# Kernel optimization log

Hardware: AMD Instinct MI355X
Metric: run time of the kernel (lower is better)

The kernel has to match this reference:

```python
import jax, jax.numpy as jnp
import numpy as np

N_NODES = 100000
IN_C, HID_C, OUT_C = 128, 128, 64
N_EDGES, N_POS, N_NEG = 1600000, 200000, 200000
BN_EPS = 1e-5


def setup_inputs() -> dict:
    key = jax.random.key(0)
    ks = jax.random.split(key, 24)
    s = 0.05
    inp = {
        'x': jax.random.normal(ks[0], (N_NODES, IN_C), jnp.float32),
        'edge_index': jax.random.randint(ks[1], (2, N_EDGES), 0, N_NODES, jnp.int64 if jax.config.jax_enable_x64 else jnp.int32),
        'pos_edge_index': jax.random.randint(ks[2], (2, N_POS), 0, N_NODES, jnp.int32),
        'neg_edge_index': jax.random.randint(ks[3], (2, N_NEG), 0, N_NODES, jnp.int32),
        # SAGEConv layer 1 (in->hid): lin_l (bias) on aggregated neighbors, lin_r (no bias) on root
        'Wl1': jax.random.normal(ks[4], (IN_C, HID_C), jnp.float32) * s,
        'bl1': jnp.zeros((HID_C,), jnp.float32),
        'Wr1': jax.random.normal(ks[5], (IN_C, HID_C), jnp.float32) * s,
        'g1': jnp.ones((HID_C,), jnp.float32),
        'b1': jnp.zeros((HID_C,), jnp.float32),
        # SAGEConv layer 2 (hid->hid)
        'Wl2': jax.random.normal(ks[6], (HID_C, HID_C), jnp.float32) * s,
        'bl2': jnp.zeros((HID_C,), jnp.float32),
        'Wr2': jax.random.normal(ks[7], (HID_C, HID_C), jnp.float32) * s,
        'g2': jnp.ones((HID_C,), jnp.float32),
        'b2': jnp.zeros((HID_C,), jnp.float32),
        # SAGEConv layer 3 (hid->out)
        'Wl3': jax.random.normal(ks[8], (HID_C, OUT_C), jnp.float32) * s,
        'bl3': jnp.zeros((OUT_C,), jnp.float32),
        'Wr3': jax.random.normal(ks[9], (HID_C, OUT_C), jnp.float32) * s,
        # edge predictor: Linear(2*out, hid) -> ReLU -> Linear(hid, 1)
        'We1': jax.random.normal(ks[10], (2 * OUT_C, HID_C), jnp.float32) * s,
        'be1': jnp.zeros((HID_C,), jnp.float32),
        'We2': jax.random.normal(ks[11], (HID_C, 1), jnp.float32) * s,
        'be2': jnp.zeros((1,), jnp.float32),
    }
    return inp


def _sage_conv(x, src, dst, Wl, bl, Wr):
    # mean aggregation of source features at destination nodes (PyG SAGEConv default)
    msg = x[src]                                                   # [E, C] gather
    agg = jax.ops.segment_sum(msg, dst, num_segments=N_NODES)      # [N, C] scatter-add
    deg = jax.ops.segment_sum(jnp.ones((src.shape[0],), x.dtype), dst, num_segments=N_NODES)
    mean = agg / jnp.maximum(deg, 1.0)[:, None]
    return mean @ Wl + bl + x @ Wr


def _bn_eval(x, gamma, beta):
    # BatchNorm1d eval mode with init running stats (mean 0, var 1)
    return x * (gamma / jnp.sqrt(1.0 + BN_EPS)) + beta


def _encode(x, edge_index, Wl1, bl1, Wr1, g1, b1, Wl2, bl2, Wr2, g2, b2, Wl3, bl3, Wr3):
    src, dst = edge_index[0], edge_index[1]
    h = x
    # layer 1 (+ residual: in_channels == hidden_channels)
    h1 = jax.nn.relu(_bn_eval(_sage_conv(h, src, dst, Wl1, bl1, Wr1), g1, b1))
    h = h1 + h if h.shape[1] == h1.shape[1] else h1
    # layer 2 (+ residual)
    h2 = jax.nn.relu(_bn_eval(_sage_conv(h, src, dst, Wl2, bl2, Wr2), g2, b2))
    h = h2 + h
    # output layer (no norm/relu/residual)
    return _sage_conv(h, src, dst, Wl3, bl3, Wr3)


def _decode(z, edge_index, We1, be1, We2, be2):
    s, d = edge_index[0], edge_index[1]
    ef = jnp.concatenate([z[s], z[d]], axis=-1)           # [E, 2*OUT_C]
    hidden = jax.nn.relu(ef @ We1 + be1)
    return jax.nn.sigmoid((hidden @ We2 + be2)[:, 0])


def reference(x, edge_index, pos_edge_index, neg_edge_index,
              Wl1, bl1, Wr1, g1, b1, Wl2, bl2, Wr2, g2, b2, Wl3, bl3, Wr3,
              We1, be1, We2, be2):
    z = _encode(x, edge_index, Wl1, bl1, Wr1, g1, b1, Wl2, bl2, Wr2, g2, b2, Wl3, bl3, Wr3)
    pos = _decode(z, pos_edge_index, We1, be1, We2, be2)
    neg = _decode(z, neg_edge_index, We1, be1, We2, be2)
    return (z, pos, neg)
```

## Files before the change

### kernel.cpp

```cpp
#include <hip/hip_runtime.h>
#include <hip/hip_bf16.h>

typedef unsigned short u16;
typedef unsigned char u8;
typedef short short8 __attribute__((ext_vector_type(8)));
typedef float floatx4 __attribute__((ext_vector_type(4)));
typedef float floatx2 __attribute__((ext_vector_type(2)));

__device__ __forceinline__ float b2f(u16 u) {
    unsigned v = ((unsigned)u) << 16;
    float f;
    __builtin_memcpy(&f, &v, 4);
    return f;
}
__device__ __forceinline__ float b2f_lo(unsigned w) { return b2f((u16)(w & 0xffffu)); }
__device__ __forceinline__ float b2f_hi(unsigned w) { return b2f((u16)(w >> 16)); }
__device__ __forceinline__ u16 f2b(float f) {
    unsigned u;
    __builtin_memcpy(&u, &f, 4);
    u = u + 0x7fffu + ((u >> 16) & 1u);
    return (u16)(u >> 16);
}
__device__ __forceinline__ unsigned pack2(float a, float b) {
    return (unsigned)f2b(a) | ((unsigned)f2b(b) << 16);
}
__device__ __forceinline__ float loadp(const void* p, int i, int f) {
    return f ? ((const float*)p)[i] : b2f(((const u16*)p)[i]);
}
__device__ __forceinline__ u8 f2e4m3(float v) {
    int r = __builtin_amdgcn_cvt_pk_fp8_f32(v, v, 0, false);
    return (u8)(r & 0xff);
}
__device__ __forceinline__ void acc16_fp8(float* a, uint4 p) {
    floatx2 f;
    f = __builtin_amdgcn_cvt_pk_f32_fp8((int)p.x, false); a[0] += f[0];  a[1] += f[1];
    f = __builtin_amdgcn_cvt_pk_f32_fp8((int)p.x, true);  a[2] += f[0];  a[3] += f[1];
    f = __builtin_amdgcn_cvt_pk_f32_fp8((int)p.y, false); a[4] += f[0];  a[5] += f[1];
    f = __builtin_amdgcn_cvt_pk_f32_fp8((int)p.y, true);  a[6] += f[0];  a[7] += f[1];
    f = __builtin_amdgcn_cvt_pk_f32_fp8((int)p.z, false); a[8] += f[0];  a[9] += f[1];
    f = __builtin_amdgcn_cvt_pk_f32_fp8((int)p.z, true);  a[10] += f[0]; a[11] += f[1];
    f = __builtin_amdgcn_cvt_pk_f32_fp8((int)p.w, false); a[12] += f[0]; a[13] += f[1];
    f = __builtin_amdgcn_cvt_pk_f32_fp8((int)p.w, true);  a[14] += f[0]; a[15] += f[1];
}

__global__ void sniff_kernel(const unsigned* __restrict__ xw, const int* __restrict__ eiw,
                             int* __restrict__ flags) {
    __shared__ int s_fp32, s_i64;
    if (threadIdx.x == 0) { s_fp32 = 0; s_i64 = 1; }
    __syncthreads();
    int t = threadIdx.x;
    unsigned w = xw[t];
    float lo = b2f_lo(w);
    if (!(fabsf(lo) <= 64.0f)) atomicOr(&s_fp32, 1);
    if (eiw[2 * t + 1] != 0) atomicAnd(&s_i64, 0);
    __syncthreads();
    if (t == 0) { flags[0] = s_fp32; flags[1] = s_i64; }
}

__global__ void cvt_x_kernel(const void* __restrict__ x, u16* __restrict__ xb,
                             u16* __restrict__ x8,
                             const int* __restrict__ flags, int nPairs) {
    int f = flags[0];
    int i = blockIdx.x * 256 + threadIdx.x;
    if (i >= nPairs) return;
    float lo, hi;
    if (f) {
        float2 v = ((const float2*)x)[i];
        lo = v.x; hi = v.y;
        ((unsigned*)xb)[i] = pack2(lo, hi);
    } else {
        unsigned w = ((const unsigned*)x)[i];
        lo = b2f_lo(w); hi = b2f_hi(w);
        ((unsigned*)xb)[i] = w;
    }
    int r = __builtin_amdgcn_cvt_pk_fp8_f32(lo, hi, 0, false);
    x8[i] = (u16)(r & 0xffff);
}

__global__ void prep_all_kernel(const void* Wl1, const void* Wr1, u16* __restrict__ Wcat1,
                                const void* Wl2, const void* Wr2, u16* __restrict__ Wcat2,
                                const void* Wl3, const void* Wr3, u16* __restrict__ Wcat3,
                                const void* We1, u16* __restrict__ Web,
                                const void* g1, const void* b1, const void* bl1,
                                float* __restrict__ al1, float* __restrict__ bt1,
                                const void* g2, const void* b2, const void* bl2,
                                float* __restrict__ al2, float* __restrict__ bt2,
                                const void* bl3,
                                float* __restrict__ al3, float* __restrict__ bt3,
                                const void* be1, const void* We2, const void* be2,
                                float* __restrict__ dparams,
                                const int* __restrict__ flags) {
    int f = flags[0];
    int idx = blockIdx.x * 256 + threadIdx.x;
    if (idx < 16384) {
        int k = idx >> 7, n = idx & 127;
        Wcat1[n * 256 + k]       = f ? f2b(((const float*)Wl1)[idx]) : ((const u16*)Wl1)[idx];
        Wcat1[n * 256 + 128 + k] = f ? f2b(((const float*)Wr1)[idx]) : ((const u16*)Wr1)[idx];
    } else if (idx < 32768) {
        int i = idx - 16384;
        int k = i >> 7, n = i & 127;
        Wcat2[n * 256 + k]       = f ? f2b(((const float*)Wl2)[i]) : ((const u16*)Wl2)[i];
        Wcat2[n * 256 + 128 + k] = f ? f2b(((const float*)Wr2)[i]) : ((const u16*)Wr2)[i];
    } else if (idx < 49152) {
        int i = idx - 32768;
        int k = i >> 7, n = i & 127;
        const void* src = (n < 64) ? Wl3 : Wr3;
        int j = k * 64 + (n & 63);
        Wcat3[n * 128 + k] = f ? f2b(((const float*)src)[j]) : ((const u16*)src)[j];
    } else if (idx < 65536) {
        int i = idx - 49152;
        int k = i >> 7, n = i & 127;
        Web[n * 128 + k] = f ? f2b(((const float*)We1)[i]) : ((const u16*)We1)[i];
    } else {
        int i = idx - 65536;
        if (i < 128) {
            float s = loadp(g1, i, f) * rsqrtf(1.0f + 1e-5f);
            al1[i] = s;
            bt1[i] = loadp(bl1, i, f) * s + loadp(b1, i, f);
        } else if (i < 256) {
            int j = i - 128;
            float s = loadp(g2, j, f) * rsqrtf(1.0f + 1e-5f);
            al2[j] = s;
            bt2[j] = loadp(bl2, j, f) * s + loadp(b2, j, f);
        } else if (i < 384) {
            int j = i - 256;
            al3[j] = 1.0f;
            bt3[j] = (j < 64) ? 0.0f : loadp(bl3, j - 64, f);
        } else if (i < 512) {
            int j = i - 384;
            dparams[j] = loadp(be1, j, f);
            dparams[128 + j] = loadp(We2, j, f);
            if (j == 0) dparams[256] = loadp(be2, 0, f);
        }
    }
}

__device__ __forceinline__ int edge_at(const int* ei, long long idx, int i64) {
    return i64 ? ei[2 * idx] : ei[idx];
}

__global__ __launch_bounds__(256) void bucket_count_kernel(const int* __restrict__ ei,
                                                           int* __restrict__ blockhist,
                                                           int E, int EPB, int nbuckP, int nbuck,
                                                           const int* __restrict__ flags) {
    __shared__ int hist[1024];
    for (int i = threadIdx.x; i < nbuck; i += 256) hist[i] = 0;
    __syncthreads();
    int i64 = flags[1];
    int b = blockIdx.x;
    int lo = b * EPB, hi = min(lo + EPB, E);
    for (int e = lo + (int)threadIdx.x; e < hi; e += 256) {
        int d = edge_at(ei, (long long)E + e, i64);
        atomicAdd(&hist[d >> 7], 1);
    }
    __syncthreads();
    for (int k = threadIdx.x; k < nbuck; k += 256)
        blockhist[(size_t)b * nbuckP + k] = hist[k];
}

__global__ __launch_bounds__(64) void colscan_kernel(int* __restrict__ blockhist,
                                                     int* __restrict__ coltot,
                                                     int B1, int nbuckP) {
    int k = blockIdx.x, l = threadIdx.x;
    int carry = 0;
    for (int base = 0; base < B1; base += 64) {
        int idx = base + l;
        int x = (idx < B1) ? blockhist[(size_t)idx * nbuckP + k] : 0;
        int s = x;
        #pragma unroll
        for (int off = 1; off < 64; off <<= 1) {
            int u = __shfl_up(s, off, 64);
            if (l >= off) s += u;
        }
        if (idx < B1) blockhist[(size_t)idx * nbuckP + k] = carry + s - x;
        carry += __shfl(s, 63, 64);
    }
    if (l == 0) coltot[k] = carry;
}

__global__ __launch_bounds__(1024) void base_scan_kernel(const int* __restrict__ coltot,
                                                         int* __restrict__ bucketbase,
                                                         int* __restrict__ rowptrN,
                                                         int nbuck, int E) {
    __shared__ int wsum[16];
    int t = threadIdx.x, lane = t & 63, w = t >> 6;
    int v = (t < nbuck) ? coltot[t] : 0;
    int inc = v;
    #pragma unroll
    for (int off = 1; off < 64; off <<= 1) {
        int u = __shfl_up(inc, off, 64);
        if (lane >= off) inc += u;
    }
    if (lane == 63) wsum[w] = inc;
    __syncthreads();
    int add = 0;
    for (int i = 0; i < w; ++i) add += wsum[i];
    if (t < nbuck) bucketbase[t] = add + inc - v;
    if (t == 0) rowptrN[0] = E;
}

__global__ __launch_bounds__(256) void bucket_scatter_kernel(const int* __restrict__ ei,
                                                             const int* __restrict__ bucketbase,
                                                             const int* __restrict__ blockhist,
                                                             unsigned* __restrict__ pairs,
                                                             int E, int EPB, int nbuckP, int nbuck,
                                                             const int* __restrict__ flags) {
    __shared__ int off[1024];
    int b = blockIdx.x;
    for (int k = threadIdx.x; k < nbuck; k += 256)
        off[k] = bucketbase[k] + blockhist[(size_t)b * nbuckP + k];
    __syncthreads();
    int i64 = flags[1];
    int lo = b * EPB, hi = min(lo + EPB, E);
    for (int e = lo + (int)threadIdx.x; e < hi; e += 256) {
        int s = edge_at(ei, e, i64);
        int d = edge_at(ei, (long long)E + e, i64);
        int slot = atomicAdd(&off[d >> 7], 1);
        pairs[slot] = (unsigned)s | ((unsigned)(d & 127) << 25);
    }
}

__global__ __launch_bounds__(256) void bucket_csr_kernel(const unsigned* __restrict__ pairs,
                                                         const int* __restrict__ bucketbase,
                                                         const int* __restrict__ coltot,
                                                         int* __restrict__ rowptr,
                                                         int* __restrict__ col, int N) {
    __shared__ unsigned pk[4096];
    __shared__ int hist[128], cur[128];
    int k = blockIdx.x, tid = threadIdx.x;
    if (tid < 128) hist[tid] = 0;
    __syncthreads();
    int base = bucketbase[k], cnt = coltot[k];
    int staged = min(cnt, 4096);
    for (int i = tid; i < cnt; i += 256) {
        unsigned pv = pairs[base + i];
        int j = (int)(pv >> 25);
        atomicAdd(&hist[j], 1);
        if (i < 4096) pk[i] = pv;
    }
    __syncthreads();
    if (tid < 64) {
        int x0 = hist[tid], x1 = hist[64 + tid];
        int s0 = x0;
        #pragma unroll
        for (int off = 1; off < 64; off <<= 1) {
            int u = __shfl_up(s0, off, 64);
            if (tid >= off) s0 += u;
        }
        int tot0 = __shfl(s0, 63, 64);
        int s1 = x1;
        #pragma unroll
        for (int off = 1; off < 64; off <<= 1) {
            int u = __shfl_up(s1, off, 64);
            if (tid >= off) s1 += u;
        }
        s1 += tot0;
        cur[tid] = s0 - x0;
        cur[64 + tid] = s1 - x1;
    }
    __syncthreads();
    int node0 = k << 7;
    if (tid < 128 && node0 + tid < N) rowptr[node0 + tid] = base + cur[tid];
    __syncthreads();
    for (int i = tid; i < staged; i += 256) {
        unsigned pv = pk[i];
        int slot = base + atomicAdd(&cur[pv >> 25], 1);
        col[slot] = (int)(pv & 0x1FFFFFFu);
    }
    for (int i = 4096 + tid; i < cnt; i += 256) {
        unsigned pv = pairs[base + i];
        int slot = base + atomicAdd(&cur[pv >> 25], 1);
        col[slot] = (int)(pv & 0x1FFFFFFu);
    }
}

template <int CH>
__global__ __launch_bounds__(256) void aggregate_fp8_kernel(const u8* __restrict__ X8,
                                                            const int* __restrict__ rowptr,
                                                            const int* __restrict__ col,
                                                            u16* __restrict__ meanout, int N) {
    constexpr int LPR = CH / 16;
    constexpr int GPB = 256 / LPR;
    int t = threadIdx.x;
    int g = t / LPR;
    int o = t % LPR;
    int u = blockIdx.x * GPB + g;
    if (u >= N) return;
    const uint4* Xv = (const uint4*)X8;
    int beg = rowptr[u], end = rowptr[u + 1];
    float a[16];
    #pragma unroll
    for (int i = 0; i < 16; ++i) a[i] = 0.f;
    int e = beg;
    for (; e + 8 <= end; e += 8) {
        uint4 p0 = Xv[(size_t)col[e]     * LPR + o];
        uint4 p1 = Xv[(size_t)col[e + 1] * LPR + o];
        uint4 p2 = Xv[(size_t)col[e + 2] * LPR + o];
        uint4 p3 = Xv[(size_t)col[e + 3] * LPR + o];
        uint4 p4 = Xv[(size_t)col[e + 4] * LPR + o];
        uint4 p5 = Xv[(size_t)col[e + 5] * LPR + o];
        uint4 p6 = Xv[(size_t)col[e + 6] * LPR + o];
        uint4 p7 = Xv[(size_t)col[e + 7] * LPR + o];
        acc16_fp8(a, p0); acc16_fp8(a, p1); acc16_fp8(a, p2); acc16_fp8(a, p3);
        acc16_fp8(a, p4); acc16_fp8(a, p5); acc16_fp8(a, p6); acc16_fp8(a, p7);
    }
    for (; e + 4 <= end; e += 4) {
        uint4 p0 = Xv[(size_t)col[e]     * LPR + o];
        uint4 p1 = Xv[(size_t)col[e + 1] * LPR + o];
        uint4 p2 = Xv[(size_t)col[e + 2] * LPR + o];
        uint4 p3 = Xv[(size_t)col[e + 3] * LPR + o];
        acc16_fp8(a, p0); acc16_fp8(a, p1); acc16_fp8(a, p2); acc16_fp8(a, p3);
    }
    for (; e < end; ++e) {
        uint4 p = Xv[(size_t)col[e] * LPR + o];
        acc16_fp8(a, p);
    }
    int deg = end - beg;
    float inv = (deg > 0) ? 1.0f / (float)deg : 0.0f;
    uint4 ov0, ov1;
    ov0.x = pack2(a[0] * inv, a[1] * inv);   ov0.y = pack2(a[2] * inv, a[3] * inv);
    ov0.z = pack2(a[4] * inv, a[5] * inv);   ov0.w = pack2(a[6] * inv, a[7] * inv);
    ov1.x = pack2(a[8] * inv, a[9] * inv);   ov1.y = pack2(a[10] * inv, a[11] * inv);
    ov1.z = pack2(a[12] * inv, a[13] * inv); ov1.w = pack2(a[14] * inv, a[15] * inv);
    uint4* mo = (uint4*)meanout;
    mo[(size_t)u * (CH / 8) + o * 2 + 0] = ov0;
    mo[(size_t)u * (CH / 8) + o * 2 + 1] = ov1;
}

__global__ __launch_bounds__(256) void agg_combine_kernel(const u8* __restrict__ T8,
                                                          const int* __restrict__ rowptr,
                                                          const int* __restrict__ col,
                                                          const u16* __restrict__ ubuf,
                                                          u16* __restrict__ zbuf,
                                                          void* __restrict__ dout,
                                                          int N, const int* __restrict__ flags) {
    constexpr int LPR = 4;
    constexpr int GPB = 64;
    int f = flags[0];
    int t = threadIdx.x;
    int g = t / LPR;
    int o = t % LPR;
    int u = blockIdx.x * GPB + g;
    if (u >= N) return;
    const uint4* Xv = (const uint4*)T8;
    int beg = rowptr[u], end = rowptr[u + 1];
    float a[16];
    #pragma unroll
    for (int i = 0; i < 16; ++i) a[i] = 0.f;
    int e = beg;
    for (; e + 8 <= end; e += 8) {
        uint4 p0 = Xv[(size_t)col[e]     * LPR + o];
        uint4 p1 = Xv[(size_t)col[e + 1] * LPR + o];
        uint4 p2 = Xv[(size_t)col[e + 2] * LPR + o];
        uint4 p3 = Xv[(size_t)col[e + 3] * LPR + o];
        uint4 p4 = Xv[(size_t)col[e + 4] * LPR + o];
        uint4 p5 = Xv[(size_t)col[e + 5] * LPR + o];
        uint4 p6 = Xv[(size_t)col[e + 6] * LPR + o];
        uint4 p7 = Xv[(size_t)col[e + 7] * LPR + o];
        acc16_fp8(a, p0); acc16_fp8(a, p1); acc16_fp8(a, p2); acc16_fp8(a, p3);
        acc16_fp8(a, p4); acc16_fp8(a, p5); acc16_fp8(a, p6); acc16_fp8(a, p7);
    }
    for (; e + 4 <= end; e += 4) {
        uint4 p0 = Xv[(size_t)col[e]     * LPR + o];
        uint4 p1 = Xv[(size_t)col[e + 1] * LPR + o];
        uint4 p2 = Xv[(size_t)col[e + 2] * LPR + o];
        uint4 p3 = Xv[(size_t)col[e + 3] * LPR + o];
        acc16_fp8(a, p0); acc16_fp8(a, p1); acc16_fp8(a, p2); acc16_fp8(a, p3);
    }
    for (; e < end; ++e) {
        uint4 p = Xv[(size_t)col[e] * LPR + o];
        acc16_fp8(a, p);
    }
    int deg = end - beg;
    float inv = (deg > 0) ? 1.0f / (float)deg : 0.0f;
    const uint4* uv = (const uint4*)(ubuf + (size_t)u * 64 + o * 16);
    uint4 u0 = uv[0], u1 = uv[1];
    float z[16];
    z[0] = a[0] * inv + b2f_lo(u0.x);  z[1] = a[1] * inv + b2f_hi(u0.x);
    z[2] = a[2] * inv + b2f_lo(u0.y);  z[3] = a[3] * inv + b2f_hi(u0.y);
    z[4] = a[4] * inv + b2f_lo(u0.z);  z[5] = a[5] * inv + b2f_hi(u0.z);
    z[6] = a[6] * inv + b2f_lo(u0.w);  z[7] = a[7] * inv + b2f_hi(u0.w);
    z[8] = a[8] * inv + b2f_lo(u1.x);  z[9] = a[9] * inv + b2f_hi(u1.x);
    z[10] = a[10] * inv + b2f_lo(u1.y); z[11] = a[11] * inv + b2f_hi(u1.y);
    z[12] = a[12] * inv + b2f_lo(u1.z); z[13] = a[13] * inv + b2f_hi(u1.z);
    z[14] = a[14] * inv + b2f_lo(u1.w); z[15] = a[15] * inv + b2f_hi(u1.w);
    uint4 zv0, zv1;
    zv0.x = pack2(z[0], z[1]);   zv0.y = pack2(z[2], z[3]);
    zv0.z = pack2(z[4], z[5]);   zv0.w = pack2(z[6], z[7]);
    zv1.x = pack2(z[8], z[9]);   zv1.y = pack2(z[10], z[11]);
    zv1.z = pack2(z[12], z[13]); zv1.w = pack2(z[14], z[15]);
    uint4* zo = (uint4*)(zbuf + (size_t)u * 64 + o * 16);
    zo[0] = zv0; zo[1] = zv1;
    if (f) {
        float* fo = (float*)dout + (size_t)u * 64 + o * 16;
        #pragma unroll
        for (int i = 0; i < 16; ++i) fo[i] = z[i];
    } else {
        uint4* bo = (uint4*)((u16*)dout + (size_t)u * 64 + o * 16);
        bo[0] = zv0; bo[1] = zv1;
    }
}

template <int K>
__global__ __launch_bounds__(256) void gemm_sage_kernel(
    const u16* __restrict__ A1, const u16* __restrict__ A2,
    const u16* __restrict__ WT,
    const float* __restrict__ alpha, const float* __restrict__ beta,
    int addRes, u16* __restrict__ out, int ldo, u16* __restrict__ outB,
    u8* __restrict__ out8, int ld8,
    int M, int relu) {
    extern __shared__ u16 As[];
    constexpr int STRIDE = K + 8;
    constexpr int NK = K / 32;
    int tid = threadIdx.x;
    int mBase = blockIdx.x * 64;
    int lane = tid & 63, w = tid >> 6;
    int q = lane >> 4, r = lane & 15;

    short8 bq[NK][2];
    {
        const u16* wr0 = WT + (size_t)(w * 32 + r) * K + q * 8;
        const u16* wr1 = WT + (size_t)(w * 32 + 16 + r) * K + q * 8;
        #pragma unroll
        for (int kk = 0; kk < NK; ++kk) {
            bq[kk][0] = *(const short8*)(wr0 + kk * 32);
            bq[kk][1] = *(const short8*)(wr1 + kk * 32);
        }
    }

    {
        int row = tid >> 2, cb = (tid & 3) * 8;
        int gr = mBase + row;
        #pragma unroll
        for (int j = 0; j < K; j += 32) {
            int k = cb + j;
            short8 v = (short8){0, 0, 0, 0, 0, 0, 0, 0};
            if (gr < M) {
                const u16* src = (k < 128) ? (A1 + (size_t)gr * 128 + k)
                                           : (A2 + (size_t)gr * 128 + (k - 128));
                v = *(const short8*)src;
            }
            *(short8*)(&As[row * STRIDE + k]) = v;
        }
    }
    __syncthreads();

    floatx4 acc[4][2];
    #pragma unroll
    for (int mi = 0; mi < 4; ++mi)
        #pragma unroll
        for (int ni = 0; ni < 2; ++ni)
            acc[mi][ni] = (floatx4){0.f, 0.f, 0.f, 0.f};

    #pragma unroll
    for (int kk = 0; kk < NK; ++kk) {
        short8 af[4];
        #pragma unroll
        for (int mi = 0; mi < 4; ++mi)
            af[mi] = *(const short8*)(&As[(mi * 16 + r) * STRIDE + kk * 32 + q * 8]);
        #pragma unroll
        for (int mi = 0; mi < 4; ++mi) {
            acc[mi][0] = __builtin_amdgcn_mfma_f32_16x16x32_bf16(af[mi], bq[kk][0], acc[mi][0], 0, 0, 0);
            acc[mi][1] = __builtin_amdgcn_mfma_f32_16x16x32_bf16(af[mi], bq[kk][1], acc[mi][1], 0, 0, 0);
        }
    }

    #pragma unroll
    for (int mi = 0; mi < 4; ++mi)
        #pragma unroll
        for (int ni = 0; ni < 2; ++ni) {
            int colv = w * 32 + ni * 16 + r;
            float al = alpha[colv], be = beta[colv];
            #pragma unroll
            for (int r4 = 0; r4 < 4; ++r4) {
                int lrow = mi * 16 + q * 4 + r4;
                int row = mBase + lrow;
                if (row < M) {
                    float v = acc[mi][ni][r4] * al + be;
                    if (relu) v = fmaxf(v, 0.0f);
                    if (K > 128 && addRes) v += b2f(As[lrow * STRIDE + 128 + colv]);
                    if (outB) {
                        if (colv < 64) out8[(size_t)row * 64 + colv] = f2e4m3(v);
                        else outB[(size_t)row * 64 + (colv - 64)] = f2b(v);
                    } else {
                        out[(size_t)row * ldo + colv] = f2b(v);
                        if (out8) out8[(size_t)row * ld8 + colv] = f2e4m3(v);
                    }
                }
            }
        }
}

__global__ __launch_bounds__(256) void decode_kernel(
    const u16* __restrict__ z,
    const int* __restrict__ pos, const int* __restrict__ neg,
    int nPos, int nNeg, int blocksPos,
    const u16* __restrict__ WebT,
    const float* __restrict__ dparams,
    void* __restrict__ dout, long long posBase,
    const int* __restrict__ flags) {
    __shared__ u16 As[64 * 136];
    __shared__ float red[4][64];
    __shared__ float be1f[128], We2f[128];
    int tid = threadIdx.x;
    int f = flags[0];
    int b = blockIdx.x;
    const int* sidx; const int* didx; int nE; long long outBase; int eBase;
    if (b < blocksPos) {
        sidx = pos; didx = pos + nPos; nE = nPos; outBase = posBase; eBase = b * 64;
    } else {
        sidx = neg; didx = neg + nNeg; nE = nNeg; outBase = posBase + nPos;
        eBase = (b - blocksPos) * 64;
    }

    int lane = tid & 63, w = tid >> 6;
    int q = lane >> 4, r = lane & 15;

    short8 zr[4];
    {
        int row = tid >> 2, ch = tid & 3;
        int e = eBase + row;
        if (e >= nE) e = nE - 1;
        int node = (ch < 2) ? sidx[e] : didx[e];
        int off = (ch & 1) * 32;
        const short8* src = (const short8*)(z + (size_t)node * 64 + off);
        #pragma unroll
        for (int j = 0; j < 4; ++j) zr[j] = src[j];
    }

    if (tid < 128) { be1f[tid] = dparams[tid]; We2f[tid] = dparams[128 + tid]; }

    short8 bfw[4][2];
    {
        const u16* w0 = WebT + (size_t)(w * 32 + r) * 128 + q * 8;
        const u16* w1 = WebT + (size_t)(w * 32 + 16 + r) * 128 + q * 8;
        #pragma unroll
        for (int kk = 0; kk < 4; ++kk) {
            bfw[kk][0] = *(const short8*)(w0 + kk * 32);
            bfw[kk][1] = *(const short8*)(w1 + kk * 32);
        }
    }

    {
        int row = tid >> 2, ch = tid & 3;
        #pragma unroll
        for (int j = 0; j < 4; ++j)
            *(short8*)(&As[row * 136 + ch * 32 + j * 8]) = zr[j];
    }
    __syncthreads();

    floatx4 acc[4][2];
    #pragma unroll
    for (int mi = 0; mi < 4; ++mi)
        #pragma unroll
        for (int ni = 0; ni < 2; ++ni)
            acc[mi][ni] = (floatx4){0.f, 0.f, 0.f, 0.f};

    #pragma unroll
    for (int kk = 0; kk < 4; ++kk) {
        short8 af[4];
        #pragma unroll
        for (int mi = 0; mi < 4; ++mi)
            af[mi] = *(const short8*)(&As[(mi * 16 + r) * 136 + kk * 32 + q * 8]);
        #pragma unroll
        for (int mi = 0; mi < 4; ++mi) {
            acc[mi][0] = __builtin_amdgcn_mfma_f32_16x16x32_bf16(af[mi], bfw[kk][0], acc[mi][0], 0, 0, 0);
            acc[mi][1] = __builtin_amdgcn_mfma_f32_16x16x32_bf16(af[mi], bfw[kk][1], acc[mi][1], 0, 0, 0);
        }
    }

    float part[4][4];
    #pragma unroll
    for (int mi = 0; mi < 4; ++mi)
        #pragma unroll
        for (int r4 = 0; r4 < 4; ++r4) part[mi][r4] = 0.f;
    #pragma unroll
    for (int mi = 0; mi < 4; ++mi)
        #pragma unroll
        for (int ni = 0; ni < 2; ++ni) {
            int colv = w * 32 + ni * 16 + r;
            float bb = be1f[colv], mm = We2f[colv];
            #pragma unroll
            for (int r4 = 0; r4 < 4; ++r4) {
                float v = acc[mi][ni][r4] + bb;
                part[mi][r4] += fmaxf(v, 0.0f) * mm;
            }
        }
    #pragma unroll
    for (int mi = 0; mi < 4; ++mi)
        #pragma unroll
        for (int r4 = 0; r4 < 4; ++r4) {
            float v = part[mi][r4];
            v += __shfl_xor(v, 1, 64);
            v += __shfl_xor(v, 2, 64);
            v += __shfl_xor(v, 4, 64);
            v += __shfl_xor(v, 8, 64);
            part[mi][r4] = v;
        }
    if (r == 0) {
        #pragma unroll
        for (int mi = 0; mi < 4; ++mi)
            #pragma unroll
            for (int r4 = 0; r4 < 4; ++r4)
                red[w][mi * 16 + q * 4 + r4] = part[mi][r4];
    }
    __syncthreads();
    if (tid < 64) {
        int e = eBase + tid;
        if (e < nE) {
            float s = red[0][tid] + red[1][tid] + red[2][tid] + red[3][tid] + dparams[256];
            float sg = 1.0f / (1.0f + expf(-s));
            if (f) ((float*)dout)[outBase + e] = sg;
            else   ((u16*)dout)[outBase + e] = f2b(sg);
        }
    }
}


extern "C" void kernel_launch(void* const* d_in, const int* in_sizes, int n_in,
                              void* d_out, int out_size, void* d_ws, size_t ws_size,
                              hipStream_t stream) {
    const void* x   = d_in[0];
    const int* ei   = (const int*)d_in[1];
    const int* pos  = (const int*)d_in[2];
    const int* neg  = (const int*)d_in[3];
    const void* Wl1 = d_in[4];
    const void* bl1 = d_in[5];
    const void* Wr1 = d_in[6];
    const void* g1  = d_in[7];
    const void* b1  = d_in[8];
    const void* Wl2 = d_in[9];
    const void* bl2 = d_in[10];
    const void* Wr2 = d_in[11];
    const void* g2  = d_in[12];
    const void* b2  = d_in[13];
    const void* Wl3 = d_in[14];
    const void* bl3 = d_in[15];
    const void* Wr3 = d_in[16];
    const void* We1 = d_in[17];
    const void* be1 = d_in[18];
    const void* We2 = d_in[19];
    const void* be2 = d_in[20];

    const int N = in_sizes[0] / 128;
    const int E = in_sizes[1] / 2;
    const int nPos = in_sizes[2] / 2;
    const int nNeg = in_sizes[3] / 2;
    const int nbuck = (N + 127) >> 7;
    const int nbuckP = (nbuck + 15) & ~15;
    const int EPB = 4096;
    const int B1 = (E + EPB - 1) / EPB;

    char* p = (char*)d_ws;
    auto alloc = [&](size_t bytes) -> void* {
        void* r = (void*)p;
        p += (bytes + 255) & ~(size_t)255;
        return r;
    };
    int*   flags     = (int*)alloc(64);
    int*   blockhist = (int*)alloc((size_t)B1 * nbuckP * 4);
    int*   coltot    = (int*)alloc((size_t)nbuck * 4);
    int*   bucketbase= (int*)alloc((size_t)nbuck * 4);
    int*   rowptr    = (int*)alloc((size_t)(N + 1) * 4);
    unsigned* pairs  = (unsigned*)alloc((size_t)E * 4);
    int*   colbuf    = (int*)alloc((size_t)E * 4);
    u16*   xb      = (u16*)alloc((size_t)N * 128 * 2);
    u16*   hbufA   = (u16*)alloc((size_t)N * 128 * 2);
    u16*   meanbuf = (u16*)alloc((size_t)N * 128 * 2);
    u8*    x8      = (u8*)alloc((size_t)N * 128);
    u8*    h8      = (u8*)alloc((size_t)N * 128);
    u8*    t8      = (u8*)alloc((size_t)N * 64);
    u16*   Wcat1   = (u16*)alloc((size_t)256 * 128 * 2);
    u16*   Wcat2   = (u16*)alloc((size_t)256 * 128 * 2);
    u16*   Wcat3   = (u16*)alloc((size_t)128 * 128 * 2);
    u16*   Web     = (u16*)alloc((size_t)128 * 128 * 2);
    float* al1 = (float*)alloc(128 * 4);
    float* bt1 = (float*)alloc(128 * 4);
    float* al2 = (float*)alloc(128 * 4);
    float* bt2 = (float*)alloc(128 * 4);
    float* al3 = (float*)alloc(128 * 4);
    float* bt3 = (float*)alloc(128 * 4);
    float* dparams = (float*)alloc(260 * 4);
    u16* hbufB = xb;
    u16* ubuf  = meanbuf + (size_t)N * 64;
    u16* zbuf  = hbufA + (size_t)N * 64;

    sniff_kernel<<<1, 256, 0, stream>>>((const unsigned*)x, ei, flags);
    bucket_count_kernel<<<B1, 256, 0, stream>>>(ei, blockhist, E, EPB, nbuckP, nbuck, flags);
    colscan_kernel<<<nbuck, 64, 0, stream>>>(blockhist, coltot, B1, nbuckP);
    base_scan_kernel<<<1, 1024, 0, stream>>>(coltot, bucketbase, rowptr + N, nbuck, E);
    bucket_scatter_kernel<<<B1, 256, 0, stream>>>(ei, bucketbase, blockhist, pairs, E, EPB, nbuckP, nbuck, flags);
    bucket_csr_kernel<<<nbuck, 256, 0, stream>>>(pairs, bucketbase, coltot, rowptr, colbuf, N);

    cvt_x_kernel<<<(N * 64 + 255) / 256, 256, 0, stream>>>(x, xb, (u16*)x8, flags, N * 64);
    prep_all_kernel<<<(66048 + 255) / 256, 256, 0, stream>>>(
        Wl1, Wr1, Wcat1, Wl2, Wr2, Wcat2, Wl3, Wr3, Wcat3, We1, Web,
        g1, b1, bl1, al1, bt1, g2, b2, bl2, al2, bt2, bl3, al3, bt3,
        be1, We2, be2, dparams, flags);

    int gB = (N + 63) / 64;
    size_t lds256 = (size_t)64 * (256 + 8) * 2;
    size_t lds128 = (size_t)64 * (128 + 8) * 2;

    aggregate_fp8_kernel<128><<<(N + 31) / 32, 256, 0, stream>>>(x8, rowptr, colbuf, meanbuf, N);
    gemm_sage_kernel<256><<<gB, 256, lds256, stream>>>(meanbuf, xb, Wcat1, al1, bt1,
                                                       1, hbufA, 128, nullptr, h8, 128, N, 1);
    aggregate_fp8_kernel<128><<<(N + 31) / 32, 256, 0, stream>>>(h8, rowptr, colbuf, meanbuf, N);
    gemm_sage_kernel<256><<<gB, 256, lds256, stream>>>(meanbuf, hbufA, Wcat2, al2, bt2,
                                                       1, hbufB, 128, nullptr, nullptr, 0, N, 1);
    gemm_sage_kernel<128><<<gB, 256, lds128, stream>>>(hbufB, hbufB, Wcat3, al3, bt3,
                                                       0, nullptr, 0, ubuf, t8, 64, N, 0);
    agg_combine_kernel<<<(N + 63) / 64, 256, 0, stream>>>(t8, rowptr, colbuf, ubuf, zbuf,
                                                          d_out, N, flags);

    long long posBase = (long long)N * 64;
    int bP = (nPos + 63) / 64, bN = (nNeg + 63) / 64;
    decode_kernel<<<bP + bN, 256, 0, stream>>>(zbuf, pos, neg, nPos, nNeg, bP,
                                               Web, dparams, d_out, posBase, flags);
}
```

Baseline: 444.6 us.

## Fuse neighbor mean aggregation into SAGE GEMM kernel via LDS staging

Replaces the separate fp8 aggregation kernel and the following GEMM for layers 1 and 2 with one kernel. Each block gathers neighbor rows, computes the mean, and writes it as bf16 straight into the shared-memory A tile, then runs the MFMA GEMM. This removes the write and re-read of the intermediate mean buffer and one launch per layer. In exchange, each block covers only 64 nodes with 4 lanes per node doing 32 channels each, which raises register use and can leave the GEMM idle while the irregular gather finishes.

```diff
diff --git a/kernel.cpp b/kernel.cpp
--- a/kernel.cpp
+++ b/kernel.cpp
@@ -274,59 +274,6 @@
     }
 }
 
-template <int CH>
-__global__ __launch_bounds__(256) void aggregate_fp8_kernel(const u8* __restrict__ X8,
-                                                            const int* __restrict__ rowptr,
-                                                            const int* __restrict__ col,
-                                                            u16* __restrict__ meanout, int N) {
-    constexpr int LPR = CH / 16;
-    constexpr int GPB = 256 / LPR;
-    int t = threadIdx.x;
-    int g = t / LPR;
-    int o = t % LPR;
-    int u = blockIdx.x * GPB + g;
-    if (u >= N) return;
-    const uint4* Xv = (const uint4*)X8;
-    int beg = rowptr[u], end = rowptr[u + 1];
-    float a[16];
-    #pragma unroll
-    for (int i = 0; i < 16; ++i) a[i] = 0.f;
-    int e = beg;
-    for (; e + 8 <= end; e += 8) {
-        uint4 p0 = Xv[(size_t)col[e]     * LPR + o];
-        uint4 p1 = Xv[(size_t)col[e + 1] * LPR + o];
-        uint4 p2 = Xv[(size_t)col[e + 2] * LPR + o];
-        uint4 p3 = Xv[(size_t)col[e + 3] * LPR + o];
-        uint4 p4 = Xv[(size_t)col[e + 4] * LPR + o];
-        uint4 p5 = Xv[(size_t)col[e + 5] * LPR + o];
-        uint4 p6 = Xv[(size_t)col[e + 6] * LPR + o];
-        uint4 p7 = Xv[(size_t)col[e + 7] * LPR + o];
-        acc16_fp8(a, p0); acc16_fp8(a, p1); acc16_fp8(a, p2); acc16_fp8(a, p3);
-        acc16_fp8(a, p4); acc16_fp8(a, p5); acc16_fp8(a, p6); acc16_fp8(a, p7);
-    }
-    for (; e + 4 <= end; e += 4) {
-        uint4 p0 = Xv[(size_t)col[e]     * LPR + o];
-        uint4 p1 = Xv[(size_t)col[e + 1] * LPR + o];
-        uint4 p2 = Xv[(size_t)col[e + 2] * LPR + o];
-        uint4 p3 = Xv[(size_t)col[e + 3] * LPR + o];
-        acc16_fp8(a, p0); acc16_fp8(a, p1); acc16_fp8(a, p2); acc16_fp8(a, p3);
-    }
-    for (; e < end; ++e) {
-        uint4 p = Xv[(size_t)col[e] * LPR + o];
-        acc16_fp8(a, p);
-    }
-    int deg = end - beg;
-    float inv = (deg > 0) ? 1.0f / (float)deg : 0.0f;
-    uint4 ov0, ov1;
-    ov0.x = pack2(a[0] * inv, a[1] * inv);   ov0.y = pack2(a[2] * inv, a[3] * inv);
-    ov0.z = pack2(a[4] * inv, a[5] * inv);   ov0.w = pack2(a[6] * inv, a[7] * inv);
-    ov1.x = pack2(a[8] * inv, a[9] * inv);   ov1.y = pack2(a[10] * inv, a[11] * inv);
-    ov1.z = pack2(a[12] * inv, a[13] * inv); ov1.w = pack2(a[14] * inv, a[15] * inv);
-    uint4* mo = (uint4*)meanout;
-    mo[(size_t)u * (CH / 8) + o * 2 + 0] = ov0;
-    mo[(size_t)u * (CH / 8) + o * 2 + 1] = ov1;
-}
-
 __global__ __launch_bounds__(256) void agg_combine_kernel(const u8* __restrict__ T8,
                                                           const int* __restrict__ rowptr,
                                                           const int* __restrict__ col,
@@ -399,6 +346,136 @@
         uint4* bo = (uint4*)((u16*)dout + (size_t)u * 64 + o * 16);
         bo[0] = zv0; bo[1] = zv1;
     }
+}
+
+__global__ __launch_bounds__(256) void fused_agg_gemm_kernel(
+    const u8* __restrict__ X8, const int* __restrict__ rowptr, const int* __restrict__ col,
+    const u16* __restrict__ A2,
+    const u16* __restrict__ WT,
+    const float* __restrict__ alpha, const float* __restrict__ beta,
+    int addRes, u16* __restrict__ out, int ldo, u16* __restrict__ outB,
+    u8* __restrict__ out8, int ld8,
+    int M, int relu) {
+    constexpr int K = 256;
+    constexpr int STRIDE = K + 8;
+    constexpr int NK = K / 32;
+    extern __shared__ u16 As[];
+    int tid = threadIdx.x;
+    int mBase = blockIdx.x * 64;
+    int lane = tid & 63, w = tid >> 6;
+    int q = lane >> 4, r = lane & 15;
+
+    {
+        int row = tid >> 2, cb = (tid & 3) * 8;
+        int gr = mBase + row;
+        #pragma unroll
+        for (int j = 128; j < 256; j += 32) {
+            int k = cb + j;
+            short8 v = (short8){0, 0, 0, 0, 0, 0, 0, 0};
+            if (gr < M) v = *(const short8*)(A2 + (size_t)gr * 128 + (k - 128));
+            *(short8*)(&As[row * STRIDE + k]) = v;
+        }
+    }
+
+    {
+        int g = tid >> 2, o = tid & 3;
+        int gr = mBase + g;
+        float a[32];
+        #pragma unroll
+        for (int i = 0; i < 32; ++i) a[i] = 0.f;
+        int beg = 0, end = 0;
+        if (gr < M) { beg = rowptr[gr]; end = rowptr[gr + 1]; }
+        const uint4* Xv = (const uint4*)X8;
+        int e = beg;
+        for (; e + 4 <= end; e += 4) {
+            size_t c0 = (size_t)col[e]     * 8 + o * 2;
+            size_t c1 = (size_t)col[e + 1] * 8 + o * 2;
+            size_t c2 = (size_t)col[e + 2] * 8 + o * 2;
+            size_t c3 = (size_t)col[e + 3] * 8 + o * 2;
+            uint4 p0a = Xv[c0], p0b = Xv[c0 + 1];
+            uint4 p1a = Xv[c1], p1b = Xv[c1 + 1];
+            uint4 p2a = Xv[c2], p2b = Xv[c2 + 1];
+            uint4 p3a = Xv[c3], p3b = Xv[c3 + 1];
+            acc16_fp8(a, p0a); acc16_fp8(a + 16, p0b);
+            acc16_fp8(a, p1a); acc16_fp8(a + 16, p1b);
+            acc16_fp8(a, p2a); acc16_fp8(a + 16, p2b);
+            acc16_fp8(a, p3a); acc16_fp8(a + 16, p3b);
+        }
+        for (; e < end; ++e) {
+            size_t c = (size_t)col[e] * 8 + o * 2;
+            uint4 pa = Xv[c], pb = Xv[c + 1];
+            acc16_fp8(a, pa); acc16_fp8(a + 16, pb);
+        }
+        int deg = end - beg;
+        float inv = (deg > 0) ? 1.0f / (float)deg : 0.0f;
+        u16* dst = &As[g * STRIDE + o * 32];
+        #pragma unroll
+        for (int j = 0; j < 4; ++j) {
+            unsigned w0 = pack2(a[j * 8 + 0] * inv, a[j * 8 + 1] * inv);
+            unsigned w1 = pack2(a[j * 8 + 2] * inv, a[j * 8 + 3] * inv);
+            unsigned w2 = pack2(a[j * 8 + 4] * inv, a[j * 8 + 5] * inv);
+            unsigned w3 = pack2(a[j * 8 + 6] * inv, a[j * 8 + 7] * inv);
+            uint4 pk4 = make_uint4(w0, w1, w2, w3);
+            *(uint4*)(dst + j * 8) = pk4;
+        }
+    }
+
+    short8 bq[NK][2];
+    {
+        const u16* wr0 = WT + (size_t)(w * 32 + r) * K + q * 8;
+        const u16* wr1 = WT + (size_t)(w * 32 + 16 + r) * K + q * 8;
+        #pragma unroll
+        for (int kk = 0; kk < NK; ++kk) {
+            bq[kk][0] = *(const short8*)(wr0 + kk * 32);
+            bq[kk][1] = *(const short8*)(wr1 + kk * 32);
+        }
+    }
+    __syncthreads();
+
+    floatx4 acc[4][2];
+    #pragma unroll
+    for (int mi = 0; mi < 4; ++mi)
+        #pragma unroll
+        for (int ni = 0; ni < 2; ++ni)
+            acc[mi][ni] = (floatx4){0.f, 0.f, 0.f, 0.f};
+
+    #pragma unroll
+    for (int kk = 0; kk < NK; ++kk) {
+        short8 af[4];
+        #pragma unroll
+        for (int mi = 0; mi < 4; ++mi)
+            af[mi] = *(const short8*)(&As[(mi * 16 + r) * STRIDE + kk * 32 + q * 8]);
+        #pragma unroll
+        for (int mi = 0; mi < 4; ++mi) {
+            acc[mi][0] = __builtin_amdgcn_mfma_f32_16x16x32_bf16(af[mi], bq[kk][0], acc[mi][0], 0, 0, 0);
+            acc[mi][1] = __builtin_amdgcn_mfma_f32_16x16x32_bf16(af[mi], bq[kk][1], acc[mi][1], 0, 0, 0);
+        }
+    }
+
+    #pragma unroll
+    for (int mi = 0; mi < 4; ++mi)
+        #pragma unroll
+        for (int ni = 0; ni < 2; ++ni) {
+            int colv = w * 32 + ni * 16 + r;
+            float al = alpha[colv], be = beta[colv];
+            #pragma unroll
+            for (int r4 = 0; r4 < 4; ++r4) {
+                int lrow = mi * 16 + q * 4 + r4;
+                int row = mBase + lrow;
+                if (row < M) {
+                    float v = acc[mi][ni][r4] * al + be;
+                    if (relu) v = fmaxf(v, 0.0f);
+                    if (addRes) v += b2f(As[lrow * STRIDE + 128 + colv]);
+                    if (outB) {
+                        if (colv < 64) out8[(size_t)row * 64 + colv] = f2e4m3(v);
+                        else outB[(size_t)row * 64 + (colv - 64)] = f2b(v);
+                    } else {
+                        out[(size_t)row * ldo + colv] = f2b(v);
+                        if (out8) out8[(size_t)row * ld8 + colv] = f2e4m3(v);
+                    }
+                }
+            }
+        }
 }
 
 template <int K>
@@ -702,12 +779,12 @@
     size_t lds256 = (size_t)64 * (256 + 8) * 2;
     size_t lds128 = (size_t)64 * (128 + 8) * 2;
 
-    aggregate_fp8_kernel<128><<<(N + 31) / 32, 256, 0, stream>>>(x8, rowptr, colbuf, meanbuf, N);
-    gemm_sage_kernel<256><<<gB, 256, lds256, stream>>>(meanbuf, xb, Wcat1, al1, bt1,
-                                                       1, hbufA, 128, nullptr, h8, 128, N, 1);
-    aggregate_fp8_kernel<128><<<(N + 31) / 32, 256, 0, stream>>>(h8, rowptr, colbuf, meanbuf, N);
-    gemm_sage_kernel<256><<<gB, 256, lds256, stream>>>(meanbuf, hbufA, Wcat2, al2, bt2,
-                                                       1, hbufB, 128, nullptr, nullptr, 0, N, 1);
+    fused_agg_gemm_kernel<<<gB, 256, lds256, stream>>>(x8, rowptr, colbuf, xb, Wcat1,
+                                                       al1, bt1, 1, hbufA, 128, nullptr,
+                                                       h8, 128, N, 1);
+    fused_agg_gemm_kernel<<<gB, 256, lds256, stream>>>(h8, rowptr, colbuf, hbufA, Wcat2,
+                                                       al2, bt2, 1, hbufB, 128, nullptr,
+                                                       nullptr, 0, N, 1);
     gemm_sage_kernel<128><<<gB, 256, lds128, stream>>>(hbufB, hbufB, Wcat3, al3, bt3,
                                                        0, nullptr, 0, ubuf, t8, 64, N, 0);
     agg_combine_kernel<<<(N + 63) / 64, 256, 0, stream>>>(t8, rowptr, colbuf, ubuf, zbuf,
```

Measured after the change: 460.3 us. 3.5% more time.
